# Optimization experiments

Hardware: AMD Instinct MI355X
Metric: run time of the kernel (lower is better)

The kernel has to match this reference:

```python
import jax, jax.numpy as jnp
import numpy as np
from jax import lax

K = 3                      # cfg.kernels
DILS = (1, 2, 4)           # dilation per learned kernel (multi-scale neighborhoods)
DMAX = 10.0                # cfg.dmax (NYUv2 max depth)
SCALES = (4, 2, 1)         # cfg.mshr_scales, coarse-to-fine
STEPS = 6                  # cfg.steps per scale
BLEND = 0.7                # cfg.mshr_blend
EDGE_TAU = 0.1             # cfg.mshr_edge_tau
EDGE_GAMMA = 1.0           # cfg.mshr_edge_gamma
ALPHA = 0.9                # cfg.anchor_alpha (fixed scalar anchor)
KAPPA_MIN, KAPPA_MAX = 0.1, 1.0
OFFSETS = ((-1,-1),(-1,0),(-1,1),(0,-1),(0,1),(1,-1),(1,0),(1,1))


def conv3(x, w, b):
    y = lax.conv_general_dilated(x, w, (1, 1), 'SAME',
                                 dimension_numbers=('NCHW', 'OIHW', 'NCHW'))
    return y + b[None, :, None, None]


def resize_bilinear(x, H, W):
    return jax.image.resize(x, (x.shape[0], x.shape[1], H, W), method='linear')


def shift2d(D, dy, dx):
    # neighbor value D[y+dy, x+dx] with zero padding outside
    py, px = abs(dy), abs(dx)
    Dp = jnp.pad(D, ((0, 0), (0, 0), (py, py), (px, px)))
    return lax.dynamic_slice(Dp, (0, 0, py + dy, px + dx), D.shape)


def gather_neighbors(D, d):
    # D: (B,1,H,W) -> (B,8,H,W) of dilated 8-neighborhood
    return jnp.concatenate([shift2d(D, dy * d, dx * d) for dy, dx in OFFSETS], axis=1)


def edge_mag(E):
    # first-difference gradient magnitude in [0,1] (matches _edge_mag_01 padding)
    gx = jnp.pad(E[..., :, 1:] - E[..., :, :-1], ((0, 0), (0, 0), (0, 0), (1, 0)))
    gy = jnp.pad(E[..., 1:, :] - E[..., :-1, :], ((0, 0), (0, 0), (1, 0), (0, 0)))
    return jnp.clip((jnp.abs(gx) + jnp.abs(gy)) * 0.5, 0.0, 1.0)


def down_sparse(DL, ML, k):
    # valid-mean pooling of sparse depth, max-pool style mask aggregation
    if k == 1:
        return DL, ML
    B, _, H, W = DL.shape
    s = (DL * ML).reshape(B, 1, H // k, k, W // k, k).sum((3, 5))
    c = ML.reshape(B, 1, H // k, k, W // k, k).sum((3, 5))
    MLs = (c > 0).astype(DL.dtype)
    DLs = jnp.where(c > 0, s / (c + 1e-6), jnp.zeros_like(s))
    return DLs, MLs


def setup_inputs() -> dict:
    key = jax.random.key(0)
    ks = jax.random.split(key, 16)
    B, H, W = 2, 480, 640
    I = jax.random.uniform(ks[0], (B, 3, H, W), dtype=jnp.float32)
    ML = (jax.random.uniform(ks[1], (B, 1, H, W)) < 0.01).astype(jnp.float32)
    DL = jax.random.uniform(ks[2], (B, 1, H, W), dtype=jnp.float32) * DMAX * ML
    E_norm = jax.random.uniform(ks[3], (B, 1, H, W), dtype=jnp.float32)
    sc = 0.1
    p = {
        'enc_w0': sc * jax.random.normal(ks[4], (64, 6, 3, 3), jnp.float32),
        'enc_b0': jnp.zeros((64,), jnp.float32),
        'enc_w1': sc * jax.random.normal(ks[5], (64, 64, 3, 3), jnp.float32),
        'enc_b1': jnp.zeros((64,), jnp.float32),
        'enc_w2': sc * jax.random.normal(ks[6], (64, 64, 3, 3), jnp.float32),
        'enc_b2': jnp.zeros((64,), jnp.float32),
        'aff_w': sc * jax.random.normal(ks[7], (K * 8, 64, 3, 3), jnp.float32),
        'aff_b': jnp.zeros((K * 8,), jnp.float32),
        'gate_w': sc * jax.random.normal(ks[8], (K, 64, 3, 3), jnp.float32),
        'gate_b': jnp.zeros((K,), jnp.float32),
        'curv_w': sc * jax.random.normal(ks[9], (K, 65, 3, 3), jnp.float32),
        'curv_b': jnp.zeros((K,), jnp.float32),
    }
    return dict(I=I, DL=DL, ML=ML, E_norm=E_norm, **p)


def _forward(I, DL, ML, E_norm, enc_w0, enc_b0, enc_w1, enc_b1, enc_w2, enc_b2,
             aff_w, aff_b, gate_w, gate_b, curv_w, curv_b):
    ML = (ML > 0).astype(jnp.float32)
    H, W = I.shape[-2], I.shape[-1]
    Dt_prev = None
    for s in SCALES:  # coarse-to-fine multi-scale hierarchy
        Hs, Ws = H // s, W // s
        I_s = resize_bilinear(I, Hs, Ws)
        E_s = jnp.clip(resize_bilinear(E_norm, Hs, Ws), 0.0, 1.0)
        DL_s, ML_s = down_sparse(DL, ML, s)
        P_s = jnp.clip(E_s * DMAX, 0.0, DMAX)  # use_poisson=False branch
        if Dt_prev is None:
            D = P_s
        else:
            up = resize_bilinear(Dt_prev, Hs, Ws)
            g = edge_mag(E_s)
            w = BLEND * jnp.clip(1.0 - g / EDGE_TAU, 0.0, 1.0) ** EDGE_GAMMA
            D = w * up + (1.0 - w) * P_s  # edge-aware blend of upsampled prev and P_s
        x = jnp.concatenate([I_s, DL_s, ML_s, E_s], axis=1)  # (B,6,Hs,Ws)
        f = jax.nn.relu(conv3(x, enc_w0, enc_b0))
        f = jax.nn.relu(conv3(f, enc_w1, enc_b1))
        feat = jax.nn.relu(conv3(f, enc_w2, enc_b2))          # (B,64,Hs,Ws)
        A = conv3(feat, aff_w, aff_b).reshape(-1, K, 8, Hs, Ws)  # learned affinities
        A = A / (jnp.sum(jnp.abs(A), axis=2, keepdims=True) + 1e-6)
        center = 1.0 - jnp.sum(A, axis=2)                      # (B,K,Hs,Ws)
        sigma = jax.nn.softmax(conv3(feat, gate_w, gate_b), axis=1)  # kernel gate
        kap_in = jnp.concatenate([feat, D / DMAX], axis=1)     # (B,65,Hs,Ws)
        kappa = KAPPA_MIN + (KAPPA_MAX - KAPPA_MIN) * jax.nn.sigmoid(conv3(kap_in, curv_w, curv_b))
        for _ in range(STEPS):  # CSPN-style anisotropic propagation
            aggs = []
            for k in range(K):
                nb = gather_neighbors(D, DILS[k])              # (B,8,Hs,Ws)
                aggs.append(center[:, k] * D[:, 0] + jnp.sum(A[:, k] * nb, axis=1))
            agg = jnp.stack(aggs, axis=1)                      # (B,K,Hs,Ws)
            mix = jnp.sum(sigma * (D + kappa * (agg - D)), axis=1, keepdims=True)
            # anchor to sparse measurements
            D = ML_s * (ALPHA * DL_s + (1.0 - ALPHA) * mix) + (1.0 - ML_s) * mix
        Dt_prev = D
    return Dt_prev  # (B,1,H,W) final metric depth


def reference(I, DL, ML, E_norm, enc_w0, enc_b0, enc_w1, enc_b1, enc_w2, enc_b2,
              aff_w, aff_b, gate_w, gate_b, curv_w, curv_b):
    return _forward(I, DL, ML, E_norm, enc_w0, enc_b0, enc_w1, enc_b1, enc_w2, enc_b2,
                    aff_w, aff_b, gate_w, gate_b, curv_w, curv_b)
```

## Files before the change

### kernel.cpp

```cpp
#include <hip/hip_runtime.h>
#include <hip/hip_bf16.h>

typedef __attribute__((ext_vector_type(8))) short short8v;
typedef __attribute__((ext_vector_type(8))) unsigned short ushort8v;
typedef __attribute__((ext_vector_type(8))) _Float16 half8v;
typedef __attribute__((ext_vector_type(4))) float f32x4;

static constexpr int BN = 2;
static constexpr int H0 = 480, W0 = 640;
static constexpr int HW1 = H0 * W0;

struct MSD {
    int s0[4], s1[4];
    int hs[3], ws[3];
    int tx0[3], tx1[3];
    unsigned long long xp8[3];
    unsigned long long x64[3];
    unsigned long long pxo[3];
};

__device__ __forceinline__ unsigned short f2h(float f) {
    _Float16 h = (_Float16)f;
    unsigned short s; __builtin_memcpy(&s, &h, 2); return s;
}
__device__ __forceinline__ float h2f(unsigned short s) {
    _Float16 h; __builtin_memcpy(&h, &s, 2); return (float)h;
}

__device__ __forceinline__ void wave_barrier() {
    asm volatile("s_waitcnt lgkmcnt(0)" ::: "memory");
    __builtin_amdgcn_sched_barrier(0);
    __builtin_amdgcn_s_barrier();
}

__global__ void wtr2_k(const float* __restrict__ w, short* __restrict__ WB) {
    int gid = blockIdx.x * 256 + threadIdx.x;
    if (gid >= 18 * 4 * 512) return;
    int ie = gid & 7;
    int l  = (gid >> 3) & 63;
    int n  = (gid >> 9) & 3;
    int t2 = gid >> 11;
    int tap = t2 >> 1, ks = t2 & 1;
    int o = 16 * n + (l & 15);
    int c = 32 * ks + (l >> 4) * 8 + ie;
    WB[gid] = (short)f2h(w[(size_t)(o * 64 + c) * 9 + tap]);
}

__global__ void wtr0_k(const float* __restrict__ w, short* __restrict__ WB) {
    int gid = blockIdx.x * 256 + threadIdx.x;
    if (gid >= 3 * 4 * 512) return;
    int ie = gid & 7;
    int l  = (gid >> 3) & 63;
    int n  = (gid >> 9) & 3;
    int j  = gid >> 11;
    int o = 16 * n + (l & 15);
    int g = l >> 4;
    int tap = 4 * j + g;
    float wv = (tap < 9 && ie < 6) ? w[(size_t)(o * 6 + ie) * 9 + tap] : 0.f;
    WB[gid] = (short)f2h(wv);
}

__global__ void whb_k(const float* __restrict__ wa, const float* __restrict__ wg,
                      const float* __restrict__ wc, short* __restrict__ WB) {
    int gid = blockIdx.x * 256 + threadIdx.x;
    if (gid >= 18 * 2 * 512) return;
    int ie = gid & 7;
    int l  = (gid >> 3) & 63;
    int n  = (gid >> 9) & 1;
    int t2 = gid >> 10;
    int tap = t2 >> 1, ks = t2 & 1;
    int o = 16 * n + (l & 15);
    int c = 32 * ks + (l >> 4) * 8 + ie;
    float wv = 0.f;
    if (o < 24)                 wv = wa[(size_t)(o * 64 + c) * 9 + tap];
    else if (o >= 24 && o < 27) wv = wg[(size_t)((o - 24) * 64 + c) * 9 + tap];
    else if (o >= 28 && o < 31) wv = wc[(size_t)((o - 28) * 65 + c) * 9 + tap];
    WB[gid] = (short)f2h(wv);
}

__global__ void hbias_k(const float* __restrict__ ba, const float* __restrict__ bg,
                        const float* __restrict__ bc, float* __restrict__ hb) {
    int o = threadIdx.x;
    if (o >= 32) return;
    float v = 0.f;
    if (o < 24) v = ba[o];
    else if (o < 27) v = bg[o - 24];
    else if (o >= 28 && o < 31) v = bc[o - 28];
    hb[o] = v;
}

template <int F>
__global__ void prep_k(const float* __restrict__ I, const float* __restrict__ DL,
                       const float* __restrict__ ML, const float* __restrict__ E,
                       short* __restrict__ Xp, float* __restrict__ Ebuf,
                       float* __restrict__ dlm, int Hs, int Ws) {
    const int pw = Ws + 2;
    int gid = blockIdx.x * 256 + threadIdx.x;
    int total = BN * (Hs + 2) * pw;
    if (gid >= total) return;
    int xp = gid % pw;
    int yp = (gid / pw) % (Hs + 2);
    int b = gid / (pw * (Hs + 2));
    short8v v = {0, 0, 0, 0, 0, 0, 0, 0};
    if (yp >= 1 && yp <= Hs && xp >= 1 && xp <= Ws) {
        int oy = yp - 1, ox = xp - 1;
        if constexpr (F == 1) {
            int p = oy * W0 + ox;
#pragma unroll
            for (int c = 0; c < 3; c++)
                v[c] = (short)f2h(I[(size_t)(b * 3 + c) * HW1 + p]);
            float e = fminf(fmaxf(E[(size_t)b * HW1 + p], 0.f), 1.f);
            v[5] = (short)f2h(e);
            Ebuf[(size_t)b * Hs * Ws + p] = e;
            float m = ML[(size_t)b * HW1 + p] > 0.f ? 1.f : 0.f;
            float s = DL[(size_t)b * HW1 + p] * m;
            float dls = m > 0.f ? s / (m + 1e-6f) : 0.f;
            v[3] = (short)f2h(dls);
            v[4] = (short)f2h(m);
            dlm[(size_t)b * Hs * Ws + p] = m > 0.f ? dls : -1.f;
        } else {
            constexpr int NT = 2 * F;
            float wy[NT], wx[NT];
            float sy = (oy + 0.5f) * F - 0.5f;
            int jly = F * oy - (F + 1) / 2;
            float wys = 0.f;
#pragma unroll
            for (int t = 0; t < NT; t++) {
                int j = jly + t;
                float w = fmaxf(1.f - fabsf(sy - (float)j) / (float)F, 0.f);
                if (j < 0 || j >= H0) w = 0.f;
                wy[t] = w; wys += w;
            }
            float sx = (ox + 0.5f) * F - 0.5f;
            int jlx = F * ox - (F + 1) / 2;
            float wxs = 0.f;
#pragma unroll
            for (int t = 0; t < NT; t++) {
                int j = jlx + t;
                float w = fmaxf(1.f - fabsf(sx - (float)j) / (float)F, 0.f);
                if (j < 0 || j >= W0) w = 0.f;
                wx[t] = w; wxs += w;
            }
            float inv = 1.f / (wys * wxs);
#pragma unroll
            for (int c = 0; c < 3; c++) {
                const float* ip = I + (size_t)(b * 3 + c) * HW1;
                float acc = 0.f;
#pragma unroll
                for (int ty = 0; ty < NT; ty++) {
                    if (wy[ty] == 0.f) continue;
                    const float* row = ip + (size_t)(jly + ty) * W0;
                    float r = 0.f;
#pragma unroll
                    for (int tx = 0; tx < NT; tx++)
                        if (wx[tx] != 0.f) r += wx[tx] * row[jlx + tx];
                    acc += wy[ty] * r;
                }
                v[c] = (short)f2h(acc * inv);
            }
            {
                const float* ip = E + (size_t)b * HW1;
                float acc = 0.f;
#pragma unroll
                for (int ty = 0; ty < NT; ty++) {
                    if (wy[ty] == 0.f) continue;
                    const float* row = ip + (size_t)(jly + ty) * W0;
                    float r = 0.f;
#pragma unroll
                    for (int tx = 0; tx < NT; tx++)
                        if (wx[tx] != 0.f) r += wx[tx] * row[jlx + tx];
                    acc += wy[ty] * r;
                }
                acc = fminf(fmaxf(acc * inv, 0.f), 1.f);
                v[5] = (short)f2h(acc);
                Ebuf[(size_t)b * Hs * Ws + oy * Ws + ox] = acc;
            }
            {
                float s = 0.f, c = 0.f;
#pragma unroll
                for (int dy = 0; dy < F; dy++)
#pragma unroll
                    for (int dx = 0; dx < F; dx++) {
                        size_t idx = ((size_t)b * H0 + (oy * F + dy)) * W0 + (ox * F + dx);
                        float m = ML[idx] > 0.f ? 1.f : 0.f;
                        s += DL[idx] * m;
                        c += m;
                    }
                float dls = c > 0.f ? s / (c + 1e-6f) : 0.f;
                v[3] = (short)f2h(dls);
                v[4] = (short)f2h(c > 0.f ? 1.f : 0.f);
                dlm[(size_t)b * Hs * Ws + oy * Ws + ox] = c > 0.f ? dls : -1.f;
            }
        }
    }
    *(short8v*)(Xp + (((size_t)b * (Hs + 6) + 2 + yp) * pw + xp) * 8) = v;
}

__global__ void dinit_first_k(const float* __restrict__ Ebuf, float* __restrict__ D0,
                              int Hs, int Ws) {
    int gid = blockIdx.x * 256 + threadIdx.x;
    int HW = Hs * Ws;
    if (gid >= BN * HW) return;
    float e = Ebuf[gid];
    D0[gid] = fminf(fmaxf(e * 10.f, 0.f), 10.f);
}

__global__ void dinit_blend_k(const float* __restrict__ Dp, const float* __restrict__ Ebuf,
                              float* __restrict__ D0, int Hs, int Ws) {
    int gid = blockIdx.x * 256 + threadIdx.x;
    int HW = Hs * Ws;
    if (gid >= BN * HW) return;
    int ox = gid % Ws;
    int oy = (gid / Ws) % Hs;
    int b = gid / HW;
    int hp = Hs / 2, wp = Ws / 2;
    const float* P = Dp + (size_t)b * hp * wp;

    float ty = 0.5f * oy - 0.25f;
    int jy = (int)floorf(ty);
    float fy = ty - jy;
    float wy0 = 1.f - fy, wy1 = fy;
    bool v0 = (jy >= 0) && (jy < hp);
    bool v1 = (jy + 1 >= 0) && (jy + 1 < hp);
    if (!v0) wy0 = 0.f;
    if (!v1) wy1 = 0.f;
    float wys = wy0 + wy1;

    float tx = 0.5f * ox - 0.25f;
    int jx = (int)floorf(tx);
    float fx = tx - jx;
    float wx0 = 1.f - fx, wx1 = fx;
    bool u0 = (jx >= 0) && (jx < wp);
    bool u1 = (jx + 1 >= 0) && (jx + 1 < wp);
    if (!u0) wx0 = 0.f;
    if (!u1) wx1 = 0.f;
    float wxs = wx0 + wx1;

    int jy0c = v0 ? jy : 0, jy1c = v1 ? (jy + 1) : 0;
    int jx0c = u0 ? jx : 0, jx1c = u1 ? (jx + 1) : 0;
    float up = wy0 * (wx0 * P[(size_t)jy0c * wp + jx0c] + wx1 * P[(size_t)jy0c * wp + jx1c])
             + wy1 * (wx0 * P[(size_t)jy1c * wp + jx0c] + wx1 * P[(size_t)jy1c * wp + jx1c]);
    up /= (wys * wxs);

    const float* Eb = Ebuf + (size_t)b * HW;
    float e = Eb[(size_t)oy * Ws + ox];
    float gx = (ox > 0) ? fabsf(e - Eb[(size_t)oy * Ws + ox - 1]) : 0.f;
    float gy = (oy > 0) ? fabsf(e - Eb[(size_t)(oy - 1) * Ws + ox]) : 0.f;
    float g = fminf(fmaxf(0.5f * (gx + gy), 0.f), 1.f);
    float w = 0.7f * fminf(fmaxf(1.f - g * 10.f, 0.f), 1.f);
    float Pv = fminf(fmaxf(e * 10.f, 0.f), 10.f);
    D0[gid] = w * up + (1.f - w) * Pv;
}

__global__ void halo0_k(short* __restrict__ A, short* __restrict__ B2, int Hs, int Ws) {
    int pw = Ws + 2;
    int ne = 2 * pw + 2 * Hs;
    int total = 4 * ne;
    int gid = blockIdx.x * 256 + threadIdx.x;
    if (gid >= total) return;
    int e = gid % ne;
    int t = gid / ne;
    int b = t & 1;
    int buf = t >> 1;
    int yp, xp;
    if (e < pw)            { yp = 0;      xp = e; }
    else if (e < 2 * pw)   { yp = Hs + 1; xp = e - pw; }
    else { int e2 = e - 2 * pw; yp = 1 + (e2 >> 1); xp = (e2 & 1) ? (Ws + 1) : 0; }
    short* p = (buf ? B2 : A) + (((size_t)b * (Hs + 6) + 2 + yp) * pw + xp) * 64;
    short8v z = {0, 0, 0, 0, 0, 0, 0, 0};
#pragma unroll
    for (int j = 0; j < 8; j++) *(short8v*)(p + j * 8) = z;
}

__device__ __forceinline__ int xcd_swz(int orig, int nwg) {
    int q = nwg >> 3, r = nwg & 7;
    int xcd = orig & 7, idx = orig >> 3;
    return (xcd < r ? xcd * (q + 1) : r * (q + 1) + (xcd - r) * q) + idx;
}

__global__ __launch_bounds__(256, 3) void conv0mm_k(
        const short* __restrict__ Xp, const short* __restrict__ WB,
        const float* __restrict__ bias, short* __restrict__ Y, MSD d) {
    const int lane = threadIdx.x & 63;
    const int wv = threadIdx.x >> 6;
    const int b = blockIdx.y;
    const int l15 = lane & 15;
    const int g = lane >> 4;
    int wg = xcd_swz(blockIdx.x, gridDim.x);
    int k = (wg >= d.s0[1]) + (wg >= d.s0[2]);
    int local = wg - d.s0[k];
    const int Hs = d.hs[k], Ws = d.ws[k], pw = Ws + 2, tX = d.tx0[k];
    int ty = local / tX, txi = local - ty * tX;
    const int y = ty * 4 + wv;
    const int x0 = txi * 64;

    const size_t bbase8 = d.xp8[k] + ((size_t)b * (Hs + 6) + 2) * pw * 8;
    const short* Xb = Xp + bbase8;

    f32x4 acc[4][4];
#pragma unroll
    for (int n = 0; n < 4; n++) {
        f32x4 bv;
#pragma unroll
        for (int j = 0; j < 4; j++) bv[j] = bias[16 * n + g * 4 + j];
#pragma unroll
        for (int cg = 0; cg < 4; cg++) acc[n][cg] = bv;
    }

    int vb[4];
#pragma unroll
    for (int cg = 0; cg < 4; cg++)
        vb[cg] = ((y + 1) * pw + (x0 + cg * 16 + l15 + 1)) * 8;

#pragma unroll
    for (int j = 0; j < 3; j++) {
        int tap = 4 * j + g;
        if (tap > 8) tap = 8;
        int toff = ((tap / 3 - 1) * pw + (tap % 3 - 1)) * 8;
        half8v bx[4];
#pragma unroll
        for (int cg = 0; cg < 4; cg++)
            bx[cg] = *(const half8v*)(Xb + vb[cg] + toff);
        const short* wp = WB + (size_t)j * (4 * 512) + lane * 8;
#pragma unroll
        for (int n = 0; n < 4; n++) {
            half8v av = *(const half8v*)(wp + n * 512);
#pragma unroll
            for (int cg = 0; cg < 4; cg++)
                acc[n][cg] = __builtin_amdgcn_mfma_f32_16x16x32_f16(
                    av, bx[cg], acc[n][cg], 0, 0, 0);
        }
    }

    const size_t bbase = d.x64[k] + ((size_t)b * (Hs + 6) + 2) * pw * 64;
#pragma unroll
    for (int cg = 0; cg < 4; cg++) {
        int x = x0 + cg * 16 + l15;
        if (x >= Ws) continue;
        short* out = Y + bbase + ((size_t)(y + 1) * pw + (x + 1)) * 64 + g * 4;
#pragma unroll
        for (int n = 0; n < 4; n++) {
            ushort4 v;
            v.x = f2h(fmaxf(acc[n][cg][0], 0.f));
            v.y = f2h(fmaxf(acc[n][cg][1], 0.f));
            v.z = f2h(fmaxf(acc[n][cg][2], 0.f));
            v.w = f2h(fmaxf(acc[n][cg][3], 0.f));
            *(ushort4*)(out + 16 * n) = v;
        }
    }
}

template <int NF, int CG, int EPI>
__global__ __launch_bounds__(256, 4) void convmm_k(
        const short* __restrict__ X, const short* __restrict__ WB,
        const float* __restrict__ bias, short* __restrict__ Y,
        unsigned short* __restrict__ cof, unsigned short* __restrict__ aux, MSD d) {
    const int lane = threadIdx.x & 63;
    const int wv = threadIdx.x >> 6;
    const int b = blockIdx.y;
    const int l15 = lane & 15;
    const int g = lane >> 4;
    int wg = xcd_swz(blockIdx.x, gridDim.x);
    int k = (wg >= d.s1[1]) + (wg >= d.s1[2]);
    int local = wg - d.s1[k];
    const int Hs = d.hs[k], Ws = d.ws[k], pw = Ws + 2, tX = d.tx1[k];
    int ty = local / tX, txi = local - ty * tX;
    const int y0r = ty * 4;
    const int y = y0r + wv;
    const int x0 = txi * (16 * CG);

    const size_t bbase = d.x64[k] + ((size_t)b * (Hs + 6) + 2) * pw * 64;
    const short* Xb = X + bbase;

    constexpr int TAPSZ = 2 * NF * 512;
    constexpr int FPW = (2 * NF) / 4;
    constexpr int C = 16 * CG + 2;
    constexpr int PCH = 72;
    __shared__ __attribute__((aligned(16))) short WL[2][TAPSZ];
    __shared__ __attribute__((aligned(16))) short XS[6 * C * PCH];

    f32x4 acc[NF][CG];
#pragma unroll
    for (int n = 0; n < NF; n++) {
        f32x4 bv;
#pragma unroll
        for (int j = 0; j < 4; j++) bv[j] = bias[16 * n + g * 4 + j];
#pragma unroll
        for (int cg = 0; cg < CG; cg++) acc[n][cg] = bv;
    }

    {
        const int total = 6 * C * 8;
        for (int c = threadIdx.x; c < total; c += 256) {
            int part = c & 7;
            int px = c >> 3;
            int row = px / C, col = px - row * C;
            short8v val = *(const short8v*)(Xb +
                ((size_t)(y0r + row) * pw + (x0 + col)) * 64 + part * 8);
            *(short8v*)(&XS[(row * C + col) * PCH + part * 8]) = val;
        }
    }
    {
        const short* src = WB + (size_t)(wv * FPW) * 512 + lane * 8;
        short* dst = &WL[0][(wv * FPW) * 512 + lane * 8];
#pragma unroll
        for (int r = 0; r < FPW; r++)
            *(short8v*)(dst + r * 512) = *(const short8v*)(src + r * 512);
    }
    wave_barrier();
    asm volatile("s_waitcnt vmcnt(0)" ::: "memory");

#pragma unroll
    for (int tap = 0; tap < 9; tap++) {
        const int cur = tap & 1;
        const int dy = tap / 3 - 1, dx = tap % 3 - 1;
        short8v stg[FPW];
        if (tap < 8) {
            const short* src = WB + (size_t)(tap + 1) * TAPSZ + (wv * FPW) * 512 + lane * 8;
#pragma unroll
            for (int r = 0; r < FPW; r++)
                stg[r] = *(const short8v*)(src + r * 512);
        }
        const int tr = wv + 1 + dy;
        half8v bx[2 * CG];
#pragma unroll
        for (int ks = 0; ks < 2; ks++)
#pragma unroll
            for (int cg = 0; cg < CG; cg++) {
                int tc = cg * 16 + l15 + 1 + dx;
                bx[ks * CG + cg] = *(const half8v*)(
                    &XS[(tr * C + tc) * PCH + ks * 32 + g * 8]);
            }
        __builtin_amdgcn_s_setprio(1);
#pragma unroll
        for (int ks = 0; ks < 2; ks++) {
            half8v wf[NF];
#pragma unroll
            for (int n = 0; n < NF; n++)
                wf[n] = *(const half8v*)(&WL[cur][(ks * NF + n) * 512 + lane * 8]);
#pragma unroll
            for (int n = 0; n < NF; n++)
#pragma unroll
                for (int cg = 0; cg < CG; cg++)
                    acc[n][cg] = __builtin_amdgcn_mfma_f32_16x16x32_f16(
                        wf[n], bx[ks * CG + cg], acc[n][cg], 0, 0, 0);
        }
        __builtin_amdgcn_s_setprio(0);
        if (tap < 8) {
            short* dst = &WL[cur ^ 1][(wv * FPW) * 512 + lane * 8];
#pragma unroll
            for (int r = 0; r < FPW; r++)
                *(short8v*)(dst + r * 512) = stg[r];
        }
        wave_barrier();
    }

    const int HW = Hs * Ws;
#pragma unroll
    for (int cg = 0; cg < CG; cg++) {
        int x = x0 + cg * 16 + l15;
        bool ok = (x < Ws);
        if (EPI == 0) {
            if (!ok) continue;
            short* out = Y + bbase + ((size_t)(y + 1) * pw + (x + 1)) * 64 + g * 4;
#pragma unroll
            for (int n = 0; n < NF; n++) {
                ushort4 v;
                v.x = f2h(fmaxf(acc[n][cg][0], 0.f));
                v.y = f2h(fmaxf(acc[n][cg][1], 0.f));
                v.z = f2h(fmaxf(acc[n][cg][2], 0.f));
                v.w = f2h(fmaxf(acc[n][cg][3], 0.f));
                *(ushort4*)(out + 16 * n) = v;
            }
        } else {
            float t0 = fabsf(acc[0][cg][0]) + fabsf(acc[0][cg][1]) +
                       fabsf(acc[0][cg][2]) + fabsf(acc[0][cg][3]);
            float s0 = t0 + __shfl_xor(t0, 16, 64);
            float t1 = fabsf(acc[1][cg][0]) + fabsf(acc[1][cg][1]) +
                       fabsf(acc[1][cg][2]) + fabsf(acc[1][cg][3]);
            float s1 = t1 + __shfl_xor(t1, 16, 64);
            float inv0 = 1.f / (s0 + 1e-6f);
            float inv1 = 1.f / (s1 + 1e-6f);
            float a0[4], a1[4];
#pragma unroll
            for (int j = 0; j < 4; j++) { a0[j] = acc[0][cg][j] * inv0; a1[j] = acc[1][cg][j] * inv1; }
            float p0 = a0[0] + a0[1] + a0[2] + a0[3];
            float c0 = p0 + __shfl_xor(p0, 16, 64);
            float p1 = a1[0] + a1[1] + a1[2] + a1[3];
            float c1 = p1 + __shfl_xor(p1, 16, 64);

            int pix = y * Ws + x;
            if (ok) {
                size_t pbase = d.pxo[k] + (size_t)b * HW + pix;
                unsigned short* cp = cof + pbase * 32;
                ushort4 va;
                va.x = f2h(a0[0]); va.y = f2h(a0[1]); va.z = f2h(a0[2]); va.w = f2h(a0[3]);
                *(ushort4*)(cp + g * 4) = va;
                if (g < 2) {
                    ushort4 vb2;
                    vb2.x = f2h(a1[0]); vb2.y = f2h(a1[1]); vb2.z = f2h(a1[2]); vb2.w = f2h(a1[3]);
                    *(ushort4*)(cp + 16 + g * 4) = vb2;
                }
                if (g == 0) {
                    cp[24] = f2h(1.f - c0);
                    cp[26] = f2h(1.f - c1);
                }
                if (g == 2) {
                    cp[25] = f2h(1.f - c0);
                    float e0 = acc[1][cg][0], e1 = acc[1][cg][1], e2 = acc[1][cg][2];
                    float m = fmaxf(e0, fmaxf(e1, e2));
                    float q0 = expf(e0 - m), q1 = expf(e1 - m), q2 = expf(e2 - m);
                    float qs = 1.f / (q0 + q1 + q2);
                    unsigned short* ap = aux + pbase * 8;
                    ap[3] = f2h(q0 * qs);
                    ap[4] = f2h(q1 * qs);
                    ap[5] = f2h(q2 * qs);
                }
                if (g == 3) {
                    unsigned short* ap = aux + pbase * 8;
                    ap[0] = f2h(acc[1][cg][0]);
                    ap[1] = f2h(acc[1][cg][1]);
                    ap[2] = f2h(acc[1][cg][2]);
                }
            }
        }
    }
}

__global__ __launch_bounds__(256) void kfix_k(const unsigned short* __restrict__ aux,
        unsigned short* __restrict__ cof, const float* __restrict__ D,
        const float* __restrict__ wc, const float* __restrict__ dlm, int Hs, int Ws) {
    int gid = blockIdx.x * 256 + threadIdx.x;
    int HW = Hs * Ws;
    if (gid >= BN * HW) return;
    int b = gid / HW;
    int p = gid - b * HW;
    int y = p / Ws;
    int x = p - y * Ws;
    const unsigned short* ap = aux + ((size_t)b * HW + p) * 8;
    float z0 = h2f(ap[0]), z1 = h2f(ap[1]), z2 = h2f(ap[2]);
    float r0 = h2f(ap[3]), r1 = h2f(ap[4]), r2 = h2f(ap[5]);
    float dsum[3] = {0.f, 0.f, 0.f};
#pragma unroll
    for (int t = 0; t < 9; t++) {
        int yy = y + t / 3 - 1;
        int xx = x + t % 3 - 1;
        if ((unsigned)yy < (unsigned)Hs && (unsigned)xx < (unsigned)Ws) {
            float dv = D[(size_t)b * HW + (size_t)yy * Ws + xx] * 0.1f;
#pragma unroll
            for (int j = 0; j < 3; j++)
                dsum[j] = fmaf(wc[(size_t)(j * 65 + 64) * 9 + t], dv, dsum[j]);
        }
    }
    unsigned short* cp = cof + ((size_t)b * HW + p) * 32;
    float zz[3] = {z0, z1, z2};
    float rr[3] = {r0, r1, r2};
#pragma unroll
    for (int j = 0; j < 3; j++) {
        float kp = 0.1f + 0.9f / (1.f + expf(-(zz[j] + dsum[j])));
        cp[27 + j] = f2h(rr[j] * kp);
    }
    float v = dlm[(size_t)b * HW + p];
    cp[30] = f2h(v >= 0.f ? v : 0.f);
    cp[31] = f2h(v >= 0.f ? 1.f : 0.f);
}

__global__ __launch_bounds__(256) void prop_k(const float* __restrict__ D,
        const unsigned short* __restrict__ cof, float* __restrict__ Dn, int Hs, int Ws) {
    int gid = blockIdx.x * 256 + threadIdx.x;
    int HW = Hs * Ws;
    if (gid >= BN * HW) return;
    int b = gid / HW;
    int p = gid - b * HW;
    int y = p / Ws;
    int x = p - y * Ws;
    const float* Db = D + (size_t)b * HW;
    float Dc = Db[p];

    const unsigned short* cp = cof + ((size_t)b * HW + p) * 32;
    ushort8v q0 = *(const ushort8v*)(cp);
    ushort8v q1 = *(const ushort8v*)(cp + 8);
    ushort8v q2 = *(const ushort8v*)(cp + 16);
    ushort8v q3 = *(const ushort8v*)(cp + 24);

    const int dy_[8] = {-1, -1, -1, 0, 0, 1, 1, 1};
    const int dx_[8] = {-1, 0, 1, -1, 1, -1, 0, 1};
    float mix = Dc;
#pragma unroll
    for (int k = 0; k < 3; k++) {
        int d = 1 << k;
        ushort8v qa = (k == 0) ? q0 : (k == 1) ? q1 : q2;
        float s = h2f(q3[k]) * Dc;
#pragma unroll
        for (int j = 0; j < 8; j++) {
            int yy = y + dy_[j] * d;
            int xx = x + dx_[j] * d;
            float nb = ((unsigned)yy < (unsigned)Hs && (unsigned)xx < (unsigned)Ws)
                           ? Db[(size_t)yy * Ws + xx] : 0.f;
            s = fmaf(h2f(qa[j]), nb, s);
        }
        mix += h2f(q3[3 + k]) * (s - Dc);
    }
    float dl = h2f(q3[6]);
    float ml = h2f(q3[7]);
    Dn[(size_t)b * HW + p] = ml * (0.9f * dl + 0.1f * mix) + (1.f - ml) * mix;
}

extern "C" void kernel_launch(void* const* d_in, const int* in_sizes, int n_in,
                              void* d_out, int out_size, void* d_ws, size_t ws_size,
                              hipStream_t stream) {
    const float* I  = (const float*)d_in[0];
    const float* DL = (const float*)d_in[1];
    const float* ML = (const float*)d_in[2];
    const float* E  = (const float*)d_in[3];
    const float* w0 = (const float*)d_in[4];  const float* b0 = (const float*)d_in[5];
    const float* w1 = (const float*)d_in[6];  const float* b1 = (const float*)d_in[7];
    const float* w2 = (const float*)d_in[8];  const float* b2 = (const float*)d_in[9];
    const float* wa = (const float*)d_in[10]; const float* ba = (const float*)d_in[11];
    const float* wg = (const float*)d_in[12]; const float* bg = (const float*)d_in[13];
    const float* wc = (const float*)d_in[14]; const float* bc = (const float*)d_in[15];

    const int hsA[3] = {120, 240, 480};
    const int wsA[3] = {160, 320, 640};
    size_t padOff[4] = {0}, xpOff[4] = {0}, pxOff[4] = {0};
    for (int k = 0; k < 3; k++) {
        size_t rows = hsA[k] + 6, cols = wsA[k] + 2;
        padOff[k + 1] = padOff[k] + (size_t)2 * rows * cols * 64;
        xpOff[k + 1]  = xpOff[k]  + (size_t)2 * rows * cols * 8;
        pxOff[k + 1]  = pxOff[k]  + (size_t)2 * hsA[k] * wsA[k];
    }

    size_t off = 0;
    auto carve = [&](size_t bytes) -> void* {
        void* pp = (char*)d_ws + off;
        off = (off + bytes + 255) & ~(size_t)255;
        return pp;
    };
    short* xpad  = (short*)carve(xpOff[3] * 2);
    float* dlm   = (float*)carve(pxOff[3] * 4);
    float* Ebuf  = (float*)carve(pxOff[3] * 4);
    float* D0    = (float*)carve((size_t)BN * HW1 * 4);
    float* D1    = (float*)carve((size_t)BN * HW1 * 4);
    float* Dprev = (float*)carve((size_t)BN * HW1 * 4);
    short* padA  = (short*)carve(padOff[3] * 2 + 65536);
    short* padB  = (short*)carve(padOff[3] * 2 + 65536);
    unsigned short* aux = (unsigned short*)padB;
    unsigned short* cof = (unsigned short*)padB + pxOff[3] * 8;
    short* WB1  = (short*)carve((size_t)18 * 4 * 512 * 2);
    short* WB2  = (short*)carve((size_t)18 * 4 * 512 * 2);
    short* WBh  = (short*)carve((size_t)18 * 2 * 512 * 2);
    short* WB0  = (short*)carve((size_t)3 * 4 * 512 * 2);
    float* hb   = (float*)carve(32 * 4);
    if (off > ws_size) return;

    MSD d;
    d.s0[0] = d.s1[0] = 0;
    for (int k = 0; k < 3; k++) {
        d.hs[k] = hsA[k]; d.ws[k] = wsA[k];
        d.tx0[k] = (wsA[k] + 63) / 64;
        d.tx1[k] = (wsA[k] + 31) / 32;
        d.s0[k + 1] = d.s0[k] + d.tx0[k] * (hsA[k] / 4);
        d.s1[k + 1] = d.s1[k] + d.tx1[k] * (hsA[k] / 4);
        d.xp8[k] = xpOff[k];
        d.x64[k] = padOff[k];
        d.pxo[k] = pxOff[k];
    }

    wtr2_k<<<(18 * 4 * 512 + 255) / 256, 256, 0, stream>>>(w1, WB1);
    wtr2_k<<<(18 * 4 * 512 + 255) / 256, 256, 0, stream>>>(w2, WB2);
    whb_k<<<(18 * 2 * 512 + 255) / 256, 256, 0, stream>>>(wa, wg, wc, WBh);
    wtr0_k<<<(3 * 4 * 512 + 255) / 256, 256, 0, stream>>>(w0, WB0);
    hbias_k<<<1, 32, 0, stream>>>(ba, bg, bc, hb);

    for (int k = 0; k < 3; k++) {
        int Hs = hsA[k], Ws = wsA[k], pw = Ws + 2;
        int nprep = (BN * (Hs + 2) * pw + 255) / 256;
        short* xpk = xpad + xpOff[k];
        float* ebk = Ebuf + pxOff[k];
        float* dlk = dlm + pxOff[k];
        if (k == 0)      prep_k<4><<<nprep, 256, 0, stream>>>(I, DL, ML, E, xpk, ebk, dlk, Hs, Ws);
        else if (k == 1) prep_k<2><<<nprep, 256, 0, stream>>>(I, DL, ML, E, xpk, ebk, dlk, Hs, Ws);
        else             prep_k<1><<<nprep, 256, 0, stream>>>(I, DL, ML, E, xpk, ebk, dlk, Hs, Ws);
        int nhalo = (4 * (2 * pw + 2 * Hs) + 255) / 256;
        halo0_k<<<nhalo, 256, 0, stream>>>(padA + padOff[k], padB + padOff[k], Hs, Ws);
    }

    conv0mm_k<<<dim3(d.s0[3], BN), 256, 0, stream>>>(xpad, WB0, b0, padA, d);
    convmm_k<4, 2, 0><<<dim3(d.s1[3], BN), 256, 0, stream>>>(padA, WB1, b1, padB,
        nullptr, nullptr, d);
    convmm_k<4, 2, 0><<<dim3(d.s1[3], BN), 256, 0, stream>>>(padB, WB2, b2, padA,
        nullptr, nullptr, d);
    convmm_k<2, 2, 1><<<dim3(d.s1[3], BN), 256, 0, stream>>>(padA, WBh, hb, nullptr,
        cof, aux, d);

    for (int si = 0; si < 3; si++) {
        int Hs = hsA[si], Ws = wsA[si], HW = Hs * Ws;
        int nbp = (BN * HW + 255) / 256;
        float* ebk = Ebuf + pxOff[si];
        float* dlk = dlm + pxOff[si];
        unsigned short* cofk = cof + pxOff[si] * 32;
        unsigned short* auxk = aux + pxOff[si] * 8;

        if (si == 0)
            dinit_first_k<<<nbp, 256, 0, stream>>>(ebk, D0, Hs, Ws);
        else
            dinit_blend_k<<<nbp, 256, 0, stream>>>(Dprev, ebk, D0, Hs, Ws);

        kfix_k<<<nbp, 256, 0, stream>>>(auxk, cofk, D0, wc, dlk, Hs, Ws);

        float* Dc = D0;
        float* Dn = D1;
        float* fin = (si < 2) ? Dprev : (float*)d_out;
        for (int t = 0; t < 6; t++) {
            float* tgt = (t == 5) ? fin : Dn;
            prop_k<<<nbp, 256, 0, stream>>>(Dc, cofk, tgt, Hs, Ws);
            if (t < 5) { float* tmp = Dc; Dc = Dn; Dn = tmp; }
        }
    }
}
```

Before: 498.2 us.

## Compute two output rows per wave in convmm to reuse weight fragments

Result: slower. 515.4 us (+3.5%).

```diff
diff --git a/kernel.cpp b/kernel.cpp
--- a/kernel.cpp
+++ b/kernel.cpp
@@ -351,7 +351,7 @@
 }
 
 template <int NF, int CG, int EPI>
-__global__ __launch_bounds__(256, 4) void convmm_k(
+__global__ __launch_bounds__(256, 2) void convmm_k(
         const short* __restrict__ X, const short* __restrict__ WB,
         const float* __restrict__ bias, short* __restrict__ Y,
         unsigned short* __restrict__ cof, unsigned short* __restrict__ aux, MSD d) {
@@ -365,8 +365,7 @@
     int local = wg - d.s1[k];
     const int Hs = d.hs[k], Ws = d.ws[k], pw = Ws + 2, tX = d.tx1[k];
     int ty = local / tX, txi = local - ty * tX;
-    const int y0r = ty * 4;
-    const int y = y0r + wv;
+    const int y0r = ty * 8;
     const int x0 = txi * (16 * CG);
 
     const size_t bbase = d.x64[k] + ((size_t)b * (Hs + 6) + 2) * pw * 64;
@@ -375,22 +374,26 @@
     constexpr int TAPSZ = 2 * NF * 512;
     constexpr int FPW = (2 * NF) / 4;
     constexpr int C = 16 * CG + 2;
-    constexpr int PCH = 72;
+    constexpr int TR = 10;
+    constexpr int PCH = 76;
     __shared__ __attribute__((aligned(16))) short WL[2][TAPSZ];
-    __shared__ __attribute__((aligned(16))) short XS[6 * C * PCH];
-
-    f32x4 acc[NF][CG];
+    __shared__ __attribute__((aligned(16))) short XS[TR * C * PCH];
+
+    f32x4 acc[NF][CG][2];
 #pragma unroll
     for (int n = 0; n < NF; n++) {
         f32x4 bv;
 #pragma unroll
         for (int j = 0; j < 4; j++) bv[j] = bias[16 * n + g * 4 + j];
 #pragma unroll
-        for (int cg = 0; cg < CG; cg++) acc[n][cg] = bv;
+        for (int cg = 0; cg < CG; cg++) {
+            acc[n][cg][0] = bv;
+            acc[n][cg][1] = bv;
+        }
     }
 
     {
-        const int total = 6 * C * 8;
+        const int total = TR * C * 8;
         for (int c = threadIdx.x; c < total; c += 256) {
             int part = c & 7;
             int px = c >> 3;
@@ -408,7 +411,6 @@
             *(short8v*)(dst + r * 512) = *(const short8v*)(src + r * 512);
     }
     wave_barrier();
-    asm volatile("s_waitcnt vmcnt(0)" ::: "memory");
 
 #pragma unroll
     for (int tap = 0; tap < 9; tap++) {
@@ -421,15 +423,18 @@
             for (int r = 0; r < FPW; r++)
                 stg[r] = *(const short8v*)(src + r * 512);
         }
-        const int tr = wv + 1 + dy;
-        half8v bx[2 * CG];
+        half8v bx[2][2][CG];
 #pragma unroll
         for (int ks = 0; ks < 2; ks++)
 #pragma unroll
-            for (int cg = 0; cg < CG; cg++) {
-                int tc = cg * 16 + l15 + 1 + dx;
-                bx[ks * CG + cg] = *(const half8v*)(
-                    &XS[(tr * C + tc) * PCH + ks * 32 + g * 8]);
+            for (int r = 0; r < 2; r++) {
+                int tr = 2 * wv + r + 1 + dy;
+#pragma unroll
+                for (int cg = 0; cg < CG; cg++) {
+                    int tc = cg * 16 + l15 + 1 + dx;
+                    bx[ks][r][cg] = *(const half8v*)(
+                        &XS[(tr * C + tc) * PCH + ks * 32 + g * 8]);
+                }
             }
         __builtin_amdgcn_s_setprio(1);
 #pragma unroll
@@ -441,9 +446,11 @@
 #pragma unroll
             for (int n = 0; n < NF; n++)
 #pragma unroll
-                for (int cg = 0; cg < CG; cg++)
-                    acc[n][cg] = __builtin_amdgcn_mfma_f32_16x16x32_f16(
-                        wf[n], bx[ks * CG + cg], acc[n][cg], 0, 0, 0);
+                for (int r = 0; r < 2; r++)
+#pragma unroll
+                    for (int cg = 0; cg < CG; cg++)
+                        acc[n][cg][r] = __builtin_amdgcn_mfma_f32_16x16x32_f16(
+                            wf[n], bx[ks][r][cg], acc[n][cg][r], 0, 0, 0);
         }
         __builtin_amdgcn_s_setprio(0);
         if (tap < 8) {
@@ -457,70 +464,77 @@
 
     const int HW = Hs * Ws;
 #pragma unroll
-    for (int cg = 0; cg < CG; cg++) {
-        int x = x0 + cg * 16 + l15;
-        bool ok = (x < Ws);
-        if (EPI == 0) {
-            if (!ok) continue;
-            short* out = Y + bbase + ((size_t)(y + 1) * pw + (x + 1)) * 64 + g * 4;
-#pragma unroll
-            for (int n = 0; n < NF; n++) {
-                ushort4 v;
-                v.x = f2h(fmaxf(acc[n][cg][0], 0.f));
-                v.y = f2h(fmaxf(acc[n][cg][1], 0.f));
-                v.z = f2h(fmaxf(acc[n][cg][2], 0.f));
-                v.w = f2h(fmaxf(acc[n][cg][3], 0.f));
-                *(ushort4*)(out + 16 * n) = v;
-            }
-        } else {
-            float t0 = fabsf(acc[0][cg][0]) + fabsf(acc[0][cg][1]) +
-                       fabsf(acc[0][cg][2]) + fabsf(acc[0][cg][3]);
-            float s0 = t0 + __shfl_xor(t0, 16, 64);
-            float t1 = fabsf(acc[1][cg][0]) + fabsf(acc[1][cg][1]) +
-                       fabsf(acc[1][cg][2]) + fabsf(acc[1][cg][3]);
-            float s1 = t1 + __shfl_xor(t1, 16, 64);
-            float inv0 = 1.f / (s0 + 1e-6f);
-            float inv1 = 1.f / (s1 + 1e-6f);
-            float a0[4], a1[4];
-#pragma unroll
-            for (int j = 0; j < 4; j++) { a0[j] = acc[0][cg][j] * inv0; a1[j] = acc[1][cg][j] * inv1; }
-            float p0 = a0[0] + a0[1] + a0[2] + a0[3];
-            float c0 = p0 + __shfl_xor(p0, 16, 64);
-            float p1 = a1[0] + a1[1] + a1[2] + a1[3];
-            float c1 = p1 + __shfl_xor(p1, 16, 64);
-
-            int pix = y * Ws + x;
-            if (ok) {
-                size_t pbase = d.pxo[k] + (size_t)b * HW + pix;
-                unsigned short* cp = cof + pbase * 32;
-                ushort4 va;
-                va.x = f2h(a0[0]); va.y = f2h(a0[1]); va.z = f2h(a0[2]); va.w = f2h(a0[3]);
-                *(ushort4*)(cp + g * 4) = va;
-                if (g < 2) {
-                    ushort4 vb2;
-                    vb2.x = f2h(a1[0]); vb2.y = f2h(a1[1]); vb2.z = f2h(a1[2]); vb2.w = f2h(a1[3]);
-                    *(ushort4*)(cp + 16 + g * 4) = vb2;
+    for (int r = 0; r < 2; r++) {
+        const int y = y0r + 2 * wv + r;
+#pragma unroll
+        for (int cg = 0; cg < CG; cg++) {
+            int x = x0 + cg * 16 + l15;
+            bool ok = (x < Ws);
+            if (EPI == 0) {
+                if (!ok) continue;
+                short* out = Y + bbase + ((size_t)(y + 1) * pw + (x + 1)) * 64 + g * 4;
+#pragma unroll
+                for (int n = 0; n < NF; n++) {
+                    ushort4 v;
+                    v.x = f2h(fmaxf(acc[n][cg][r][0], 0.f));
+                    v.y = f2h(fmaxf(acc[n][cg][r][1], 0.f));
+                    v.z = f2h(fmaxf(acc[n][cg][r][2], 0.f));
+                    v.w = f2h(fmaxf(acc[n][cg][r][3], 0.f));
+                    *(ushort4*)(out + 16 * n) = v;
                 }
-                if (g == 0) {
-                    cp[24] = f2h(1.f - c0);
-                    cp[26] = f2h(1.f - c1);
+            } else {
+                float t0 = fabsf(acc[0][cg][r][0]) + fabsf(acc[0][cg][r][1]) +
+                           fabsf(acc[0][cg][r][2]) + fabsf(acc[0][cg][r][3]);
+                float s0 = t0 + __shfl_xor(t0, 16, 64);
+                float t1 = fabsf(acc[1][cg][r][0]) + fabsf(acc[1][cg][r][1]) +
+                           fabsf(acc[1][cg][r][2]) + fabsf(acc[1][cg][r][3]);
+                float s1 = t1 + __shfl_xor(t1, 16, 64);
+                float inv0 = 1.f / (s0 + 1e-6f);
+                float inv1 = 1.f / (s1 + 1e-6f);
+                float a0[4], a1[4];
+#pragma unroll
+                for (int j = 0; j < 4; j++) {
+                    a0[j] = acc[0][cg][r][j] * inv0;
+                    a1[j] = acc[1][cg][r][j] * inv1;
                 }
-                if (g == 2) {
-                    cp[25] = f2h(1.f - c0);
-                    float e0 = acc[1][cg][0], e1 = acc[1][cg][1], e2 = acc[1][cg][2];
-                    float m = fmaxf(e0, fmaxf(e1, e2));
-                    float q0 = expf(e0 - m), q1 = expf(e1 - m), q2 = expf(e2 - m);
-                    float qs = 1.f / (q0 + q1 + q2);
-                    unsigned short* ap = aux + pbase * 8;
-                    ap[3] = f2h(q0 * qs);
-                    ap[4] = f2h(q1 * qs);
-                    ap[5] = f2h(q2 * qs);
-                }
-                if (g == 3) {
-                    unsigned short* ap = aux + pbase * 8;
-                    ap[0] = f2h(acc[1][cg][0]);
-                    ap[1] = f2h(acc[1][cg][1]);
-                    ap[2] = f2h(acc[1][cg][2]);
+                float p0 = a0[0] + a0[1] + a0[2] + a0[3];
+                float c0 = p0 + __shfl_xor(p0, 16, 64);
+                float p1 = a1[0] + a1[1] + a1[2] + a1[3];
+                float c1 = p1 + __shfl_xor(p1, 16, 64);
+
+                int pix = y * Ws + x;
+                if (ok) {
+                    size_t pbase = d.pxo[k] + (size_t)b * HW + pix;
+                    unsigned short* cp = cof + pbase * 32;
+                    ushort4 va;
+                    va.x = f2h(a0[0]); va.y = f2h(a0[1]); va.z = f2h(a0[2]); va.w = f2h(a0[3]);
+                    *(ushort4*)(cp + g * 4) = va;
+                    if (g < 2) {
+                        ushort4 vb2;
+                        vb2.x = f2h(a1[0]); vb2.y = f2h(a1[1]); vb2.z = f2h(a1[2]); vb2.w = f2h(a1[3]);
+                        *(ushort4*)(cp + 16 + g * 4) = vb2;
+                    }
+                    if (g == 0) {
+                        cp[24] = f2h(1.f - c0);
+                        cp[26] = f2h(1.f - c1);
+                    }
+                    if (g == 2) {
+                        cp[25] = f2h(1.f - c0);
+                        float e0 = acc[1][cg][r][0], e1 = acc[1][cg][r][1], e2 = acc[1][cg][r][2];
+                        float m = fmaxf(e0, fmaxf(e1, e2));
+                        float q0 = expf(e0 - m), q1 = expf(e1 - m), q2 = expf(e2 - m);
+                        float qs = 1.f / (q0 + q1 + q2);
+                        unsigned short* ap = aux + pbase * 8;
+                        ap[3] = f2h(q0 * qs);
+                        ap[4] = f2h(q1 * qs);
+                        ap[5] = f2h(q2 * qs);
+                    }
+                    if (g == 3) {
+                        unsigned short* ap = aux + pbase * 8;
+                        ap[0] = f2h(acc[1][cg][r][0]);
+                        ap[1] = f2h(acc[1][cg][r][1]);
+                        ap[2] = f2h(acc[1][cg][r][2]);
+                    }
                 }
             }
         }
@@ -660,7 +674,7 @@
         d.tx0[k] = (wsA[k] + 63) / 64;
         d.tx1[k] = (wsA[k] + 31) / 32;
         d.s0[k + 1] = d.s0[k] + d.tx0[k] * (hsA[k] / 4);
-        d.s1[k + 1] = d.s1[k] + d.tx1[k] * (hsA[k] / 4);
+        d.s1[k + 1] = d.s1[k] + d.tx1[k] * (hsA[k] / 8);
         d.xp8[k] = xpOff[k];
         d.x64[k] = padOff[k];
         d.pxo[k] = pxOff[k];
```
